# Kernel tuning notes

Hardware: AMD Instinct MI355X
Metric: run time of the kernel (lower is better)

Reference implementation:

```python
import jax, jax.numpy as jnp
import numpy as np


def setup_inputs() -> dict:
    key = jax.random.key(0)
    k1, k2 = jax.random.split(key)
    B, C, L, K = 32, 64, 4096, 512
    inputs = jax.random.normal(k1, (B, C, L), dtype=jnp.float32)
    # codebook init: uniform(-1/K, 1/K) as in the torch module
    embed = jax.random.uniform(k2, (K, C), dtype=jnp.float32, minval=-1.0 / K, maxval=1.0 / K)
    return {"inputs": inputs, "embed": embed}


def reference(inputs, embed):
    commitment_cost = 0.25
    b, c, l = inputs.shape
    K = embed.shape[0]
    # (B, C, L) -> (B*L, C)
    flat = jnp.transpose(inputs, (0, 2, 1)).reshape(-1, c)
    flat_sq = jnp.sum(flat * flat, axis=1, keepdims=True)            # (N, 1)
    embed_sq = jnp.sum(embed * embed, axis=1)                        # (K,)
    distances = flat_sq + embed_sq[None, :] - 2.0 * (flat @ embed.T)  # (N, K)
    encoding_indices = jnp.argmin(distances, axis=1)                 # (N,)
    encodings = jax.nn.one_hot(encoding_indices, K, dtype=flat.dtype)  # (N, K)
    # gather codewords (equivalent to one_hot @ embed) and restore (B, C, L)
    quantized = jnp.transpose(embed[encoding_indices].reshape(b, l, c), (0, 2, 1))
    e_latent_loss = jnp.mean((jax.lax.stop_gradient(quantized) - inputs) ** 2)
    q_latent_loss = jnp.mean((quantized - jax.lax.stop_gradient(inputs)) ** 2)
    loss = q_latent_loss + commitment_cost * e_latent_loss
    # straight-through estimator
    quantized_st = inputs + jax.lax.stop_gradient(quantized - inputs)
    avg_probs = jnp.mean(encodings, axis=0)                          # (K,)
    perplexity = jnp.exp(-jnp.sum(avg_probs * jnp.log(avg_probs + 1e-10)))
    return (loss, quantized_st, perplexity, embed, encoding_indices.reshape(b, l), encodings)
```

## Files before the change

kernel.cpp:

```cpp
#include <hip/hip_runtime.h>
#include <math.h>

#define B_DIM 32
#define C_DIM 64
#define L_DIM 4096
#define K_CB  512
#define N_ROWS (B_DIM * L_DIM)
#define Q_ELEMS (B_DIM * C_DIM * L_DIM)

#define OFF_LOSS  0
#define OFF_Q     1
#define OFF_PERP  (1 + Q_ELEMS)
#define OFF_EMBED (OFF_PERP + 1)
#define OFF_IDX   (OFF_EMBED + K_CB * C_DIM)
#define OFF_ENC   (OFF_IDX + N_ROWS)

#define TM 128
#define KC 64

using f4 = __attribute__((ext_vector_type(4))) float;
using f2 = __attribute__((ext_vector_type(2))) float;


__global__ void vq_init(const float* __restrict__ embed,
                        double* __restrict__ loss_ws,
                        int* __restrict__ hist,
                        float* __restrict__ esq,
                        float* __restrict__ out_embed) {
  const int t = threadIdx.x;
  if (t == 0) *loss_ws = 0.0;
  hist[t] = 0;
  const float* row = embed + (size_t)t * C_DIM;
  float s = 0.f;
#pragma unroll
  for (int c = 0; c < C_DIM; ++c) s = fmaf(row[c], row[c], s);
  esq[t] = s;
#pragma unroll
  for (int i = 0; i < K_CB * C_DIM / 512; ++i)
    out_embed[i * 512 + t] = embed[i * 512 + t];
}

__global__ __launch_bounds__(256) void vq_fused(
    const float* __restrict__ in, const float* __restrict__ embed,
    const float* __restrict__ esq_g, int* __restrict__ hist,
    double* __restrict__ loss_ws, float* __restrict__ out) {
  __shared__ float xT[C_DIM][TM];
  __shared__ float eT[KC][C_DIM];
  __shared__ int   idx_s[TM];
  __shared__ double red[256];

  const int tid = threadIdx.x;
  const int blk = blockIdx.x;
  const int b   = blk >> 5;
  const int l0  = (blk & 31) * TM;
  const float* xbase = in + (size_t)b * C_DIM * L_DIM + l0;

  {
    const int rr = (tid & 31) * 4;
    const int c0 = tid >> 5;
#pragma unroll
    for (int p = 0; p < 8; ++p) {
      const int c = c0 * 8 + p;
      const f4 v = *(const f4*)(xbase + (size_t)c * L_DIM + rr);
      *(f4*)&xT[c][rr] = v;
    }
  }

  const int cg  = (tid & 15) * 4;
  const int kk0 = tid >> 4;
  f4 pf[4];
#pragma unroll
  for (int p = 0; p < 4; ++p)
    pf[p] = *(const f4*)(embed + (size_t)(kk0 + p * 16) * C_DIM + cg);

  __syncthreads();

  const int tx = tid & 15;
  const int ty = tid >> 4;

  float* fsq_tmp = &eT[0][0];
  if (tid < TM) {
    float s = 0.f;
#pragma unroll
    for (int c = 0; c < C_DIM; ++c) { const float v = xT[c][tid]; s = fmaf(v, v, s); }
    fsq_tmp[tid] = s;
  }
  __syncthreads();
  float fs[8];
#pragma unroll
  for (int i = 0; i < 8; ++i) fs[i] = fsq_tmp[ty * 8 + i];

  const int swz = tx << 2;
  float rmin[8];
  int   ridx[8];
#pragma unroll
  for (int i = 0; i < 8; ++i) { rmin[i] = 3.402823466e38f; ridx[i] = 0; }

  for (int kc = 0; kc < K_CB / KC; ++kc) {
    const int k0 = kc * KC;
    __syncthreads();
#pragma unroll
    for (int p = 0; p < 4; ++p) {
      const int kk = kk0 + p * 16;
      const int cs = cg ^ (((kk >> 2) & 15) << 2);
      *(f4*)&eT[kk][cs] = pf[p];
    }
    if (kc < K_CB / KC - 1) {
#pragma unroll
      for (int p = 0; p < 4; ++p)
        pf[p] = *(const f4*)(embed + (size_t)(k0 + KC + kk0 + p * 16) * C_DIM + cg);
    }
    float qe[4];
#pragma unroll
    for (int j = 0; j < 4; ++j) qe[j] = esq_g[k0 + tx * 4 + j];
    __syncthreads();

    float acc[8][4];
#pragma unroll
    for (int i = 0; i < 8; ++i)
#pragma unroll
      for (int j = 0; j < 4; ++j) acc[i][j] = 0.f;

#pragma unroll 2
    for (int c = 0; c < C_DIM; c += 4) {
      f4 xa[4], xb[4], ev[4];
#pragma unroll
      for (int cc = 0; cc < 4; ++cc) {
        xa[cc] = *(const f4*)&xT[c + cc][ty * 8];
        xb[cc] = *(const f4*)&xT[c + cc][ty * 8 + 4];
      }
      const int cb = c ^ swz;
#pragma unroll
      for (int j = 0; j < 4; ++j)
        ev[j] = *(const f4*)&eT[tx * 4 + j][cb];
#pragma unroll
      for (int cc = 0; cc < 4; ++cc) {
#pragma unroll
        for (int j = 0; j < 4; ++j) {
          const float e = ev[j][cc];
#pragma unroll
          for (int i = 0; i < 4; ++i) acc[i][j]     = fmaf(xa[cc][i], e, acc[i][j]);
#pragma unroll
          for (int i = 0; i < 4; ++i) acc[i + 4][j] = fmaf(xb[cc][i], e, acc[i + 4][j]);
        }
      }
    }

#pragma unroll
    for (int i = 0; i < 8; ++i) {
#pragma unroll
      for (int j = 0; j < 4; ++j) {
        const float d = fmaf(-2.0f, acc[i][j], fs[i] + qe[j]);
        const int k = k0 + tx * 4 + j;
        if (d < rmin[i]) { rmin[i] = d; ridx[i] = k; }
      }
    }
  }

#pragma unroll
  for (int off = 8; off; off >>= 1) {
#pragma unroll
    for (int i = 0; i < 8; ++i) {
      const float od = __shfl_xor(rmin[i], off, 16);
      const int   oi = __shfl_xor(ridx[i], off, 16);
      if (od < rmin[i] || (od == rmin[i] && oi < ridx[i])) { rmin[i] = od; ridx[i] = oi; }
    }
  }

  if (tx == 0) {
#pragma unroll
    for (int i = 0; i < 8; ++i) idx_s[ty * 8 + i] = ridx[i];
  }
  __syncthreads();

  if (tid < TM) {
    const int k = idx_s[tid];
    out[OFF_IDX + blk * TM + tid] = (float)k;
    atomicAdd(&hist[k], 1);
  }

  double ls = 0.0;
  {
    float* eSel = &eT[0][0];
    float* qbase = out + OFF_Q + (size_t)b * (C_DIM * L_DIM) + l0;
    const int cc = tid & 63;
    const int w  = tid >> 6;
#pragma unroll
    for (int pass = 0; pass < 2; ++pass) {
      const int r0 = pass * 64;
      __syncthreads();
#pragma unroll 4
      for (int it = 0; it < 16; ++it) {
        const int r = it * 4 + w;
        const int k = idx_s[r0 + r];
        eSel[r * C_DIM + (cc ^ (r & 31))] = embed[(size_t)k * C_DIM + cc];
      }
      __syncthreads();
#pragma unroll 4
      for (int it = 0; it < 16; ++it) {
        const int f = it * 256 + tid;
        const int c = f >> 6;
        const int r = f & 63;
        const float x = xT[c][r0 + r];
        const float q = eSel[r * C_DIM + (c ^ (r & 31))];
        const float d = q - x;
        __builtin_nontemporal_store(x + d, qbase + (size_t)c * L_DIM + r0 + r);
        ls += (double)(d * d);
      }
    }
  }

  {
    f2* enc = (f2*)(out + OFF_ENC) + (size_t)blk * TM * (K_CB / 2);
#pragma unroll 4
    for (int it = 0; it < TM; ++it) {
      const int k = idx_s[it];
      const int j2 = tid << 1;
      f2 v;
      v.x = (j2 == k)     ? 1.0f : 0.0f;
      v.y = (j2 + 1 == k) ? 1.0f : 0.0f;
      __builtin_nontemporal_store(v, enc + it * 256 + tid);
    }
  }

  red[tid] = ls;
  __syncthreads();
  for (int s = 128; s; s >>= 1) {
    if (tid < s) red[tid] += red[tid + s];
    __syncthreads();
  }
  if (tid == 0) atomicAdd(loss_ws, red[0]);
}

__global__ void vq_final(const int* __restrict__ hist, const double* __restrict__ loss_ws,
                         float* __restrict__ out) {
  __shared__ float red[512];
  const int t = threadIdx.x;
  const float p = (float)hist[t] * (1.0f / (float)N_ROWS);
  red[t] = p * logf(p + 1e-10f);
  __syncthreads();
  for (int s = 256; s; s >>= 1) {
    if (t < s) red[t] += red[t + s];
    __syncthreads();
  }
  if (t == 0) {
    out[OFF_PERP] = expf(-red[0]);
    const float m = (float)(*loss_ws / (double)Q_ELEMS);
    out[OFF_LOSS] = m + 0.25f * m;
  }
}

extern "C" void kernel_launch(void* const* d_in, const int* in_sizes, int n_in,
                              void* d_out, int out_size, void* d_ws, size_t ws_size,
                              hipStream_t stream) {
  (void)in_sizes; (void)n_in; (void)out_size; (void)ws_size;
  const float* in    = (const float*)d_in[0];
  const float* embed = (const float*)d_in[1];
  float* out = (float*)d_out;

  double* loss_ws = (double*)d_ws;
  int*    hist    = (int*)((char*)d_ws + 16);
  float*  esq     = (float*)((char*)d_ws + 4096);

  vq_init<<<1, 512, 0, stream>>>(embed, loss_ws, hist, esq, out + OFF_EMBED);
  vq_fused<<<N_ROWS / TM, 256, 0, stream>>>(in, embed, esq, hist, loss_ws, out);
  vq_final<<<1, 512, 0, stream>>>(hist, loss_ws, out);
}
```

Before: 167.6 us.

## Replace LDS-tiled distance GEMM with per-thread row kept in registers

The shared-memory tiled distance computation (8x4 register tile per thread, staged and swizzled codebook chunks) is replaced by a scheme with one row per thread. Each thread holds its 64-element input vector in registers and reads the codebook directly from global memory, four codewords at a time. Because all threads in a wavefront read the same codebook address, those loads become broadcast or scalar, which removes LDS traffic and most barriers. The trade-offs are much lower arithmetic reuse per load, higher register pressure, 128-thread blocks, and input rows reloaded from global memory in the epilogue, and the per-block argmin tie-breaking changes.

```diff
diff --git a/kernel.cpp b/kernel.cpp
--- a/kernel.cpp
+++ b/kernel.cpp
@@ -15,10 +15,8 @@
 #define OFF_IDX   (OFF_EMBED + K_CB * C_DIM)
 #define OFF_ENC   (OFF_IDX + N_ROWS)
 
-#define TM 128
-#define KC 64
+#define RPB 128
 
-using f4 = __attribute__((ext_vector_type(4))) float;
 using f2 = __attribute__((ext_vector_type(2))) float;
 
 
@@ -40,148 +38,59 @@
     out_embed[i * 512 + t] = embed[i * 512 + t];
 }
 
-__global__ __launch_bounds__(256) void vq_fused(
+__global__ __launch_bounds__(128) void vq_fused(
     const float* __restrict__ in, const float* __restrict__ embed,
     const float* __restrict__ esq_g, int* __restrict__ hist,
     double* __restrict__ loss_ws, float* __restrict__ out) {
-  __shared__ float xT[C_DIM][TM];
-  __shared__ float eT[KC][C_DIM];
-  __shared__ int   idx_s[TM];
-  __shared__ double red[256];
+  __shared__ float  eSel[64 * C_DIM];
+  __shared__ int    idx_s[RPB];
+  __shared__ double red[RPB];
 
   const int tid = threadIdx.x;
   const int blk = blockIdx.x;
   const int b   = blk >> 5;
-  const int l0  = (blk & 31) * TM;
-  const float* xbase = in + (size_t)b * C_DIM * L_DIM + l0;
+  const int l0  = (blk & 31) * RPB;
+  const int l   = l0 + tid;
 
-  {
-    const int rr = (tid & 31) * 4;
-    const int c0 = tid >> 5;
+  const float* xp = in + (size_t)b * (C_DIM * L_DIM) + l;
+  float x[C_DIM];
 #pragma unroll
-    for (int p = 0; p < 8; ++p) {
-      const int c = c0 * 8 + p;
-      const f4 v = *(const f4*)(xbase + (size_t)c * L_DIM + rr);
-      *(f4*)&xT[c][rr] = v;
+  for (int c = 0; c < C_DIM; ++c) x[c] = xp[(size_t)c * L_DIM];
+
+  float fs = 0.f;
+#pragma unroll
+  for (int c = 0; c < C_DIM; ++c) fs = fmaf(x[c], x[c], fs);
+
+  float rmin = 3.402823466e38f;
+  int   ridx = 0;
+  for (int g = 0; g < K_CB / 4; ++g) {
+    const float* e0 = embed + (size_t)g * 4 * C_DIM;
+    float a0 = 0.f, a1 = 0.f, a2 = 0.f, a3 = 0.f;
+#pragma unroll
+    for (int c = 0; c < C_DIM; ++c) {
+      const float xv = x[c];
+      a0 = fmaf(xv, e0[c], a0);
+      a1 = fmaf(xv, e0[C_DIM + c], a1);
+      a2 = fmaf(xv, e0[2 * C_DIM + c], a2);
+      a3 = fmaf(xv, e0[3 * C_DIM + c], a3);
     }
+    const int k0 = g * 4;
+    const float d0 = fmaf(-2.0f, a0, fs + esq_g[k0 + 0]);
+    if (d0 < rmin) { rmin = d0; ridx = k0 + 0; }
+    const float d1 = fmaf(-2.0f, a1, fs + esq_g[k0 + 1]);
+    if (d1 < rmin) { rmin = d1; ridx = k0 + 1; }
+    const float d2 = fmaf(-2.0f, a2, fs + esq_g[k0 + 2]);
+    if (d2 < rmin) { rmin = d2; ridx = k0 + 2; }
+    const float d3 = fmaf(-2.0f, a3, fs + esq_g[k0 + 3]);
+    if (d3 < rmin) { rmin = d3; ridx = k0 + 3; }
   }
 
-  const int cg  = (tid & 15) * 4;
-  const int kk0 = tid >> 4;
-  f4 pf[4];
-#pragma unroll
-  for (int p = 0; p < 4; ++p)
-    pf[p] = *(const f4*)(embed + (size_t)(kk0 + p * 16) * C_DIM + cg);
-
-  __syncthreads();
-
-  const int tx = tid & 15;
-  const int ty = tid >> 4;
-
-  float* fsq_tmp = &eT[0][0];
-  if (tid < TM) {
-    float s = 0.f;
-#pragma unroll
-    for (int c = 0; c < C_DIM; ++c) { const float v = xT[c][tid]; s = fmaf(v, v, s); }
-    fsq_tmp[tid] = s;
-  }
-  __syncthreads();
-  float fs[8];
-#pragma unroll
-  for (int i = 0; i < 8; ++i) fs[i] = fsq_tmp[ty * 8 + i];
-
-  const int swz = tx << 2;
-  float rmin[8];
-  int   ridx[8];
-#pragma unroll
-  for (int i = 0; i < 8; ++i) { rmin[i] = 3.402823466e38f; ridx[i] = 0; }
-
-  for (int kc = 0; kc < K_CB / KC; ++kc) {
-    const int k0 = kc * KC;
-    __syncthreads();
-#pragma unroll
-    for (int p = 0; p < 4; ++p) {
-      const int kk = kk0 + p * 16;
-      const int cs = cg ^ (((kk >> 2) & 15) << 2);
-      *(f4*)&eT[kk][cs] = pf[p];
-    }
-    if (kc < K_CB / KC - 1) {
-#pragma unroll
-      for (int p = 0; p < 4; ++p)
-        pf[p] = *(const f4*)(embed + (size_t)(k0 + KC + kk0 + p * 16) * C_DIM + cg);
-    }
-    float qe[4];
-#pragma unroll
-    for (int j = 0; j < 4; ++j) qe[j] = esq_g[k0 + tx * 4 + j];
-    __syncthreads();
-
-    float acc[8][4];
-#pragma unroll
-    for (int i = 0; i < 8; ++i)
-#pragma unroll
-      for (int j = 0; j < 4; ++j) acc[i][j] = 0.f;
-
-#pragma unroll 2
-    for (int c = 0; c < C_DIM; c += 4) {
-      f4 xa[4], xb[4], ev[4];
-#pragma unroll
-      for (int cc = 0; cc < 4; ++cc) {
-        xa[cc] = *(const f4*)&xT[c + cc][ty * 8];
-        xb[cc] = *(const f4*)&xT[c + cc][ty * 8 + 4];
-      }
-      const int cb = c ^ swz;
-#pragma unroll
-      for (int j = 0; j < 4; ++j)
-        ev[j] = *(const f4*)&eT[tx * 4 + j][cb];
-#pragma unroll
-      for (int cc = 0; cc < 4; ++cc) {
-#pragma unroll
-        for (int j = 0; j < 4; ++j) {
-          const float e = ev[j][cc];
-#pragma unroll
-          for (int i = 0; i < 4; ++i) acc[i][j]     = fmaf(xa[cc][i], e, acc[i][j]);
-#pragma unroll
-          for (int i = 0; i < 4; ++i) acc[i + 4][j] = fmaf(xb[cc][i], e, acc[i + 4][j]);
-        }
-      }
-    }
-
-#pragma unroll
-    for (int i = 0; i < 8; ++i) {
-#pragma unroll
-      for (int j = 0; j < 4; ++j) {
-        const float d = fmaf(-2.0f, acc[i][j], fs[i] + qe[j]);
-        const int k = k0 + tx * 4 + j;
-        if (d < rmin[i]) { rmin[i] = d; ridx[i] = k; }
-      }
-    }
-  }
-
-#pragma unroll
-  for (int off = 8; off; off >>= 1) {
-#pragma unroll
-    for (int i = 0; i < 8; ++i) {
-      const float od = __shfl_xor(rmin[i], off, 16);
-      const int   oi = __shfl_xor(ridx[i], off, 16);
-      if (od < rmin[i] || (od == rmin[i] && oi < ridx[i])) { rmin[i] = od; ridx[i] = oi; }
-    }
-  }
-
-  if (tx == 0) {
-#pragma unroll
-    for (int i = 0; i < 8; ++i) idx_s[ty * 8 + i] = ridx[i];
-  }
-  __syncthreads();
-
-  if (tid < TM) {
-    const int k = idx_s[tid];
-    out[OFF_IDX + blk * TM + tid] = (float)k;
-    atomicAdd(&hist[k], 1);
-  }
+  out[OFF_IDX + blk * RPB + tid] = (float)ridx;
+  atomicAdd(&hist[ridx], 1);
+  idx_s[tid] = ridx;
 
   double ls = 0.0;
   {
-    float* eSel = &eT[0][0];
     float* qbase = out + OFF_Q + (size_t)b * (C_DIM * L_DIM) + l0;
     const int cc = tid & 63;
     const int w  = tid >> 6;
@@ -190,42 +99,51 @@
       const int r0 = pass * 64;
       __syncthreads();
 #pragma unroll 4
-      for (int it = 0; it < 16; ++it) {
-        const int r = it * 4 + w;
+      for (int it = 0; it < 32; ++it) {
+        const int r = it * 2 + w;
         const int k = idx_s[r0 + r];
         eSel[r * C_DIM + (cc ^ (r & 31))] = embed[(size_t)k * C_DIM + cc];
       }
       __syncthreads();
 #pragma unroll 4
-      for (int it = 0; it < 16; ++it) {
-        const int f = it * 256 + tid;
+      for (int it = 0; it < 32; ++it) {
+        const int f = it * 128 + tid;
         const int c = f >> 6;
         const int r = f & 63;
-        const float x = xT[c][r0 + r];
-        const float q = eSel[r * C_DIM + (c ^ (r & 31))];
-        const float d = q - x;
-        __builtin_nontemporal_store(x + d, qbase + (size_t)c * L_DIM + r0 + r);
+        const float xx = in[(size_t)b * (C_DIM * L_DIM) + (size_t)c * L_DIM + l0 + r0 + r];
+        const float q  = eSel[r * C_DIM + (c ^ (r & 31))];
+        const float d  = q - xx;
+        __builtin_nontemporal_store(xx + d, qbase + (size_t)c * L_DIM + r0 + r);
         ls += (double)(d * d);
       }
     }
   }
 
   {
-    f2* enc = (f2*)(out + OFF_ENC) + (size_t)blk * TM * (K_CB / 2);
+    f2* enc = (f2*)(out + OFF_ENC) + (size_t)blk * RPB * (K_CB / 2);
 #pragma unroll 4
-    for (int it = 0; it < TM; ++it) {
+    for (int it = 0; it < RPB; ++it) {
       const int k = idx_s[it];
-      const int j2 = tid << 1;
-      f2 v;
-      v.x = (j2 == k)     ? 1.0f : 0.0f;
-      v.y = (j2 + 1 == k) ? 1.0f : 0.0f;
-      __builtin_nontemporal_store(v, enc + it * 256 + tid);
+      {
+        const int j2 = tid << 1;
+        f2 v;
+        v.x = (j2 == k)     ? 1.0f : 0.0f;
+        v.y = (j2 + 1 == k) ? 1.0f : 0.0f;
+        __builtin_nontemporal_store(v, enc + it * 256 + tid);
+      }
+      {
+        const int j2 = (tid + 128) << 1;
+        f2 v;
+        v.x = (j2 == k)     ? 1.0f : 0.0f;
+        v.y = (j2 + 1 == k) ? 1.0f : 0.0f;
+        __builtin_nontemporal_store(v, enc + it * 256 + 128 + tid);
+      }
     }
   }
 
   red[tid] = ls;
   __syncthreads();
-  for (int s = 128; s; s >>= 1) {
+  for (int s = 64; s; s >>= 1) {
     if (tid < s) red[tid] += red[tid + s];
     __syncthreads();
   }
@@ -263,6 +181,6 @@
   float*  esq     = (float*)((char*)d_ws + 4096);
 
   vq_init<<<1, 512, 0, stream>>>(embed, loss_ws, hist, esq, out + OFF_EMBED);
-  vq_fused<<<N_ROWS / TM, 256, 0, stream>>>(in, embed, esq, hist, loss_ws, out);
+  vq_fused<<<N_ROWS / RPB, RPB, 0, stream>>>(in, embed, esq, hist, loss_ws, out);
   vq_final<<<1, 512, 0, stream>>>(hist, loss_ws, out);
 }
```

Result: slower. 376.7 us (+124.7%).
